# Kernel optimization log

Measured on AMD Instinct MI355X. Metric: run time of the kernel, lower is better.

The kernel has to match this reference:

```python
import jax, jax.numpy as jnp
import numpy as np

B, L, DN, DE, DD, H = 2, 512, 512, 128, 128, 8
DK, DEH, DDH = DN // H, DE // H, DD // H
F = 2 * DK + DEH + 2 * DDH  # per-head concat feature size (176)
SLOPE = 0.2


def _kaiming(key, out_f, in_f):
    bound = np.sqrt(6.0 / ((1.0 + SLOPE ** 2) * in_f))
    return jax.random.uniform(key, (out_f, in_f), minval=-bound, maxval=bound, dtype=jnp.float32)


def lin(x, w, b):
    y = jnp.einsum('...i,oi->...o', x, w)
    return y if b is None else y + b


def setup_inputs() -> dict:
    key = jax.random.key(0)
    ks = jax.random.split(key, 16)
    inp = {
        'node_representation': jax.random.normal(ks[0], (B, L, DN), dtype=jnp.float32),
        'edge_representation': jax.random.normal(ks[1], (B, L, L, DE), dtype=jnp.float32),
        'diff_vec': jax.random.normal(ks[2], (B, L, DD), dtype=jnp.float32),
        'Wn_w': _kaiming(ks[3], DN, DN), 'Wn_b': jnp.zeros((DN,), jnp.float32),
        'We_w': _kaiming(ks[4], DE, DE), 'We_b': jnp.zeros((DE,), jnp.float32),
        'Wd_w': _kaiming(ks[5], DD, DD), 'Wd_b': jnp.zeros((DD,), jnp.float32),
        'Wh_w': _kaiming(ks[6], DK, DK), 'Wh_b': jnp.zeros((DK,), jnp.float32),
        'attn_w': _kaiming(ks[7], 1, F),
        'outn_w': _kaiming(ks[8], DN, DN), 'outn_b': jnp.zeros((DN,), jnp.float32),
        'Wn2_w': _kaiming(ks[9], DN, DN), 'Wn2_b': jnp.zeros((DN,), jnp.float32),
        'We2_w': _kaiming(ks[10], DE, DE), 'We2_b': jnp.zeros((DE,), jnp.float32),
        'Wd2_w': _kaiming(ks[11], DD, DD), 'Wd2_b': jnp.zeros((DD,), jnp.float32),
        'edge_w': _kaiming(ks[12], DEH, F), 'edge_b': jnp.zeros((DEH,), jnp.float32),
        'oute_w': _kaiming(ks[13], DE, DE), 'oute_b': jnp.zeros((DE,), jnp.float32),
    }
    return inp


def reference(node_representation, edge_representation, diff_vec,
              Wn_w, Wn_b, We_w, We_b, Wd_w, Wd_b, Wh_w, Wh_b, attn_w,
              outn_w, outn_b, Wn2_w, Wn2_b, We2_w, We2_b, Wd2_w, Wd2_b,
              edge_w, edge_b, oute_w, oute_b):
    lrelu = lambda x: jax.nn.leaky_relu(x, SLOPE)

    # ---- node update (GAT-style with concat score decomposed per term) ----
    npj = lin(node_representation, Wn_w, Wn_b).reshape(B, L, H, DK)
    epj = lin(edge_representation, We_w, We_b).reshape(B, L, L, H, DEH)
    dpj = lin(diff_vec, Wd_w, Wd_b).reshape(B, L, H, DDH)
    a = attn_w[0]  # concat order: [hi, hj, edge, di, dj]
    a_hi, a_hj = a[:DK], a[DK:2 * DK]
    a_e = a[2 * DK:2 * DK + DEH]
    a_di, a_dj = a[2 * DK + DEH:2 * DK + DEH + DDH], a[-DDH:]
    # scores[b,i,j,h]
    s = (jnp.einsum('blhd,d->blh', npj, a_hi)[:, :, None, :]
         + jnp.einsum('blhd,d->blh', npj, a_hj)[:, None, :, :]
         + jnp.einsum('blmhe,e->blmh', epj, a_e)
         + jnp.einsum('blhd,d->blh', dpj, a_di)[:, :, None, :]
         + jnp.einsum('blhd,d->blh', dpj, a_dj)[:, None, :, :])
    diag = jnp.eye(L, dtype=bool)[None, :, :, None]
    s = jnp.where(diag, -jnp.inf, s)
    probs = jax.nn.softmax(lrelu(s), axis=2)  # softmax over j
    node_wh = lin(npj, Wh_w, Wh_b)  # [B,L,H,DK]
    agg = jnp.einsum('blmh,bmhd->blhd', probs, node_wh)
    new_node = (npj + lrelu(agg)).reshape(B, L, DN)
    new_node = lin(new_node, outn_w, outn_b)

    # ---- edge update (concat-linear decomposed into per-term matmuls) ----
    np2 = lin(new_node, Wn2_w, Wn2_b).reshape(B, L, H, DK)
    ep2 = lin(edge_representation, We2_w, We2_b).reshape(B, L, L, H, DEH)
    dp2 = lin(diff_vec, Wd2_w, Wd2_b).reshape(B, L, H, DDH)
    # edge concat order: [edge, hi, hj, di, dj]
    W_e = edge_w[:, :DEH]
    W_hi = edge_w[:, DEH:DEH + DK]
    W_hj = edge_w[:, DEH + DK:DEH + 2 * DK]
    W_di = edge_w[:, DEH + 2 * DK:DEH + 2 * DK + DDH]
    W_dj = edge_w[:, -DDH:]
    e_out = (jnp.einsum('blmhe,fe->blmhf', ep2, W_e)
             + jnp.einsum('blhd,fd->blhf', np2, W_hi)[:, :, None]
             + jnp.einsum('blhd,fd->blhf', np2, W_hj)[:, None]
             + jnp.einsum('blhd,fd->blhf', dp2, W_di)[:, :, None]
             + jnp.einsum('blhd,fd->blhf', dp2, W_dj)[:, None]
             + edge_b)
    new_edge = lin(e_out.reshape(B, L, L, DE), oute_w, oute_b)
    return new_node, new_edge
```

## Files before the change

kernel.cpp:

```cpp
#include <hip/hip_runtime.h>
#include <hip/hip_bf16.h>

typedef unsigned short u16;
typedef unsigned short u16x8 __attribute__((ext_vector_type(8)));
typedef __bf16 bf16x8 __attribute__((ext_vector_type(8)));
typedef float f32x4 __attribute__((ext_vector_type(4)));

#define LRS 0.2f

__device__ __forceinline__ float bf2f(u16 u) { return __uint_as_float(((unsigned)u) << 16); }
__device__ __forceinline__ u16 f2b(float f) {
  __hip_bfloat16 h = __float2bfloat16(f);
  return __builtin_bit_cast(u16, h);
}

template<int K, int O, int KSEG>
__device__ __forceinline__ void gemm_rows4(const float* xr, const float* W, const float* bias,
                                           float* yl, float* yg, int ygstride) {
  constexpr int KPT = K / KSEG;
  constexpr int OPP = 256 / KSEG;
  const int t = threadIdx.x;
  const int ks = t % KSEG;
  const int oi = t / KSEG;
#pragma unroll
  for (int pass = 0; pass < O / OPP; ++pass) {
    const int o = pass * OPP + oi;
    float a0 = 0, a1 = 0, a2 = 0, a3 = 0;
    const float* wp = W + (size_t)o * K + ks * KPT;
    const float* xb = xr + ks * KPT;
#pragma unroll 4
    for (int kc = 0; kc < KPT; kc += 4) {
      f32x4 w4 = *(const f32x4*)(wp + kc);
      f32x4 x0 = *(const f32x4*)(xb + kc);
      f32x4 x1 = *(const f32x4*)(xb + K + kc);
      f32x4 x2 = *(const f32x4*)(xb + 2 * K + kc);
      f32x4 x3 = *(const f32x4*)(xb + 3 * K + kc);
#pragma unroll
      for (int j = 0; j < 4; ++j) {
        float w = w4[j];
        a0 += x0[j] * w;
        a1 += x1[j] * w;
        a2 += x2[j] * w;
        a3 += x3[j] * w;
      }
    }
#pragma unroll
    for (int d = 1; d < KSEG; d <<= 1) {
      a0 += __shfl_xor(a0, d, 64);
      a1 += __shfl_xor(a1, d, 64);
      a2 += __shfl_xor(a2, d, 64);
      a3 += __shfl_xor(a3, d, 64);
    }
    if (ks == 0) {
      float bv = bias ? bias[o] : 0.0f;
      float v0 = a0 + bv, v1 = a1 + bv, v2 = a2 + bv, v3 = a3 + bv;
      if (yl) { yl[o] = v0; yl[O + o] = v1; yl[2 * O + o] = v2; yl[3 * O + o] = v3; }
      if (yg) { yg[o] = v0; yg[ygstride + o] = v1; yg[2 * (size_t)ygstride + o] = v2; yg[3 * (size_t)ygstride + o] = v3; }
    }
  }
}

__global__ __launch_bounds__(256) void kW1(const float* We_w, const float* We_b, const float* attn,
                                           const float* We2_w, const float* We2_b,
                                           const float* edge_w, const float* edge_b,
                                           float* Mfull, float* vf, float* cbe, float* sconst) {
  int gid = blockIdx.x * 256 + threadIdx.x;
  if (gid < 16384) {
    int hf = gid >> 7, c = gid & 127;
    int h = hf >> 4, fo = hf & 15;
    float s = 0;
    for (int e = 0; e < 16; ++e)
      s += edge_w[fo * 176 + e] * We2_w[(h * 16 + e) * 128 + c];
    Mfull[hf * 128 + c] = s;
  } else if (gid < 16384 + 2048) {
    int idx = gid - 16384;
    int c = idx >> 4, hc = idx & 15;
    if (hc < 8) {
      float s = 0;
      for (int e = 0; e < 16; ++e)
        s += We_w[(hc * 16 + e) * 128 + c] * attn[128 + e];
      vf[c * 8 + hc] = s;
    }
  } else if (gid < 18432 + 128) {
    int hf = gid - 18432;
    int h = hf >> 4, fo = hf & 15;
    float s = edge_b[fo];
    for (int e = 0; e < 16; ++e)
      s += We2_b[h * 16 + e] * edge_w[fo * 176 + e];
    cbe[hf] = s;
  } else if (gid < 18560 + 8) {
    int h = gid - 18560;
    float s = 0;
    for (int e = 0; e < 16; ++e)
      s += We_b[h * 16 + e] * attn[128 + e];
    sconst[h] = s;
  }
}

__global__ __launch_bounds__(256) void kW2(const float* oute_w, const float* Mfull, u16* Gb) {
  int gid = blockIdx.x * 256 + threadIdx.x;
  int o = gid >> 7, c = gid & 127;
  float s = 0;
  for (int k = 0; k < 128; ++k)
    s += oute_w[o * 128 + k] * Mfull[k * 128 + c];
  Gb[o * 128 + c] = f2b(s);
}

__global__ __launch_bounds__(256) void kN1(const float* node, const float* diff,
                                           const float* Wn_w, const float* Wn_b,
                                           const float* Wd_w, const float* Wd_b,
                                           const float* Wh_w, const float* Wh_b,
                                           const float* attn, const float* sconst,
                                           float* npj_g, float* nwh_g,
                                           float* srow_g, float* scol_g) {
  __shared__ float nrow[4 * 512], npjl[4 * 512], drow[4 * 128], dpjl[4 * 128];
  const int t = threadIdx.x;
  const int r0 = blockIdx.x * 4;
  *(f32x4*)&nrow[t * 8]     = *(const f32x4*)(node + (size_t)r0 * 512 + t * 8);
  *(f32x4*)&nrow[t * 8 + 4] = *(const f32x4*)(node + (size_t)r0 * 512 + t * 8 + 4);
  if (t < 64) {
    *(f32x4*)&drow[t * 8]     = *(const f32x4*)(diff + (size_t)r0 * 128 + t * 8);
    *(f32x4*)&drow[t * 8 + 4] = *(const f32x4*)(diff + (size_t)r0 * 128 + t * 8 + 4);
  }
  __syncthreads();
  gemm_rows4<512, 512, 4>(nrow, Wn_w, Wn_b, npjl, npj_g + (size_t)r0 * 512, 512);
  gemm_rows4<128, 128, 4>(drow, Wd_w, Wd_b, dpjl, nullptr, 0);
  __syncthreads();
  {
    int d = t & 63, hh = t >> 6;
#pragma unroll
    for (int hi = 0; hi < 2; ++hi) {
      int h = hh + hi * 4;
      float wb = Wh_b[d];
      float acc[4] = {wb, wb, wb, wb};
      for (int k = 0; k < 64; ++k) {
        float w = Wh_w[d * 64 + k];
#pragma unroll
        for (int r = 0; r < 4; ++r) acc[r] += npjl[r * 512 + h * 64 + k] * w;
      }
#pragma unroll
      for (int r = 0; r < 4; ++r) nwh_g[(size_t)(r0 + r) * 512 + h * 64 + d] = acc[r];
    }
  }
  if (t < 32) {
    int r = t >> 3, h = t & 7;
    float shi = 0, shj = 0, sdi = 0, sdj = 0;
    for (int d = 0; d < 64; ++d) {
      float x = npjl[r * 512 + h * 64 + d];
      shi += x * attn[d];
      shj += x * attn[64 + d];
    }
    for (int e = 0; e < 16; ++e) {
      float x = dpjl[r * 128 + h * 16 + e];
      sdi += x * attn[144 + e];
      sdj += x * attn[160 + e];
    }
    srow_g[(r0 + r) * 8 + h] = shi + sdi + sconst[h];
    scol_g[(r0 + r) * 8 + h] = shj + sdj;
  }
}

__global__ __launch_bounds__(256) void kA(const float* edge, const float* npj, const float* nwh,
                                          const float* srow, const float* scol,
                                          const float* vf, float* nnp) {
  __shared__ float sm[4608];
  __shared__ u16 Pb[4][512][8];
  __shared__ float red[256];
  __shared__ float mxh8[8];
  __shared__ float inv8v[4][8];
  const int blk = blockIdx.x;
  const int b = blk >> 7, lt = blk & 127;
  const int t = threadIdx.x;
  const int sub = t & 15, rg = t >> 4;
  const int h = t & 7, seg = t >> 3;

  f32x4 vrx[16];
#pragma unroll
  for (int q = 0; q < 16; ++q) vrx[q] = *(const f32x4*)(vf + sub * 64 + q * 4);

  for (int li = 0; li < 4; ++li) {
    const int l = lt * 4 + li;
    const size_t bl = (size_t)b * 512 + l;
    const float* ebase = edge + (bl * 512 + rg) * 128 + sub * 8;
    f32x4 a0v, a1v, b0v, b1v;
    a0v = *(const f32x4*)ebase;             a1v = *(const f32x4*)(ebase + 4);
    b0v = *(const f32x4*)(ebase + 2048);    b1v = *(const f32x4*)(ebase + 2052);
#define SCORE_ROW(C0, C1, IT)                                                  \
    {                                                                          \
      float acc[8];                                                            \
      _Pragma("unroll") for (int h2 = 0; h2 < 8; ++h2) acc[h2] = 0.0f;         \
      _Pragma("unroll") for (int j = 0; j < 4; ++j) {                          \
        _Pragma("unroll") for (int h2 = 0; h2 < 8; ++h2) {                     \
          acc[h2] += C0[j] * vrx[j * 2 + (h2 >> 2)][h2 & 3];                   \
          acc[h2] += C1[j] * vrx[8 + j * 2 + (h2 >> 2)][h2 & 3];               \
        }                                                                      \
      }                                                                        \
      _Pragma("unroll") for (int d = 1; d < 16; d <<= 1) {                     \
        _Pragma("unroll") for (int h2 = 0; h2 < 8; ++h2)                       \
          acc[h2] += __shfl_xor(acc[h2], d, 64);                               \
      }                                                                        \
      if (sub < 8) {                                                           \
        float a = acc[0];                                                      \
        _Pragma("unroll") for (int h2 = 1; h2 < 8; ++h2)                       \
          if (sub == h2) a = acc[h2];                                          \
        sm[(IT * 16 + rg) * 9 + sub] = a;                                      \
      }                                                                        \
    }
    for (int it = 0; it < 32; it += 2) {
      SCORE_ROW(a0v, a1v, it);
      if (it + 2 < 32) {
        const float* p = ebase + (size_t)(it + 2) * 2048;
        a0v = *(const f32x4*)p; a1v = *(const f32x4*)(p + 4);
      }
      SCORE_ROW(b0v, b1v, (it + 1));
      if (it + 3 < 32) {
        const float* p = ebase + (size_t)(it + 3) * 2048;
        b0v = *(const f32x4*)p; b1v = *(const f32x4*)(p + 4);
      }
    }
#undef SCORE_ROW
    __syncthreads();
    const float srh2 = srow[bl * 8 + h];
    float mx = -__builtin_inff();
#pragma unroll 4
    for (int i = 0; i < 16; ++i) {
      int m = seg * 16 + i;
      float sv = sm[m * 9 + h] + srh2 + scol[((size_t)b * 512 + m) * 8 + h];
      sv = (m == l) ? -__builtin_inff() : (sv >= 0.0f ? sv : LRS * sv);
      sm[m * 9 + h] = sv;
      mx = fmaxf(mx, sv);
    }
    red[t] = mx;
    __syncthreads();
    if (t < 8) {
      float m2 = -__builtin_inff();
      for (int sg = 0; sg < 32; ++sg) m2 = fmaxf(m2, red[sg * 8 + t]);
      mxh8[t] = m2;
    }
    __syncthreads();
    float mh = mxh8[h];
    float smv = 0;
#pragma unroll 4
    for (int i = 0; i < 16; ++i) {
      int m = seg * 16 + i;
      float p = __expf(sm[m * 9 + h] - mh);
      Pb[li][m][h] = f2b(p);
      smv += p;
    }
    red[t] = smv;
    __syncthreads();
    if (t < 8) {
      float s2 = 0;
      for (int sg = 0; sg < 32; ++sg) s2 += red[sg * 8 + t];
      inv8v[li][t] = 1.0f / s2;
    }
    __syncthreads();
  }

  const int half = t >> 7, oq = t & 127;
  const int o4 = oq * 4, hh = oq >> 4;
  f32x4 acc[4] = {};
  const float* nb = nwh + (size_t)b * 512 * 512;
  for (int m = half * 256; m < half * 256 + 256; ++m) {
    f32x4 nv = *(const f32x4*)(nb + (size_t)m * 512 + o4);
#pragma unroll
    for (int li = 0; li < 4; ++li)
      acc[li] += bf2f(Pb[li][m][hh]) * nv;
  }
#pragma unroll
  for (int li = 0; li < 4; ++li)
    *(f32x4*)&sm[(half * 4 + li) * 512 + o4] = acc[li];
  __syncthreads();
  if (t < 128) {
    int ob = t * 4, h2 = t >> 4;
#pragma unroll
    for (int li = 0; li < 4; ++li) {
      f32x4 s0 = *(f32x4*)&sm[li * 512 + ob];
      f32x4 s1 = *(f32x4*)&sm[(4 + li) * 512 + ob];
      const size_t bl = (size_t)b * 512 + lt * 4 + li;
      f32x4 np4 = *(const f32x4*)(npj + bl * 512 + ob);
      float iv = inv8v[li][h2];
      f32x4 o;
#pragma unroll
      for (int j = 0; j < 4; ++j) {
        float a = (s0[j] + s1[j]) * iv;
        a = a >= 0.0f ? a : LRS * a;
        o[j] = np4[j] + a;
      }
      *(f32x4*)(nnp + bl * 512 + ob) = o;
    }
  }
}

__global__ __launch_bounds__(256) void kN2(const float* nnp, const float* outn_w, const float* outn_b,
                                           float* out0) {
  __shared__ float xr[4 * 512];
  const int t = threadIdx.x;
  const int r0 = blockIdx.x * 4;
  *(f32x4*)&xr[t * 4]        = *(const f32x4*)(nnp + (size_t)r0 * 512 + t * 4);
  *(f32x4*)&xr[1024 + t * 4] = *(const f32x4*)(nnp + (size_t)r0 * 512 + 1024 + t * 4);
  __syncthreads();
  gemm_rows4<512, 512, 4>(xr, outn_w, outn_b, nullptr, out0 + (size_t)r0 * 512, 512);
}

__global__ __launch_bounds__(256) void kN34(const float* nn, const float* diff,
                                            const float* Wn2_w, const float* Wn2_b,
                                            const float* Wd2_w, const float* Wd2_b,
                                            const float* edge_w, const float* cbe,
                                            const float* oute_w, const float* oute_b,
                                            float* Pl, float* Pm) {
  __shared__ float xr[4 * 512], np2l[4 * 512], dr[4 * 128], dp2l[4 * 128];
  __shared__ float Rls[4 * 128], Rms[4 * 128];
  const int t = threadIdx.x;
  const int r0 = blockIdx.x * 4;
  *(f32x4*)&xr[t * 4]        = *(const f32x4*)(nn + (size_t)r0 * 512 + t * 4);
  *(f32x4*)&xr[1024 + t * 4] = *(const f32x4*)(nn + (size_t)r0 * 512 + 1024 + t * 4);
  if (t < 64) {
    *(f32x4*)&dr[t * 8]     = *(const f32x4*)(diff + (size_t)r0 * 128 + t * 8);
    *(f32x4*)&dr[t * 8 + 4] = *(const f32x4*)(diff + (size_t)r0 * 128 + t * 8 + 4);
  }
  __syncthreads();
  gemm_rows4<512, 512, 4>(xr, Wn2_w, Wn2_b, np2l, nullptr, 0);
  gemm_rows4<128, 128, 4>(dr, Wd2_w, Wd2_b, dp2l, nullptr, 0);
  __syncthreads();
  {
    int hf = t & 127, which = t >> 7;
    int h = hf >> 4, fo = hf & 15;
    const float* wh = edge_w + fo * 176 + 16 + which * 64;
    const float* wd = edge_w + fo * 176 + 144 + which * 16;
    float add = which ? 0.0f : cbe[hf];
    float* dst = which ? Rms : Rls;
#pragma unroll
    for (int r = 0; r < 4; ++r) {
      float a = add;
      for (int d = 0; d < 64; ++d) a += np2l[r * 512 + h * 64 + d] * wh[d];
      for (int e = 0; e < 16; ++e) a += dp2l[r * 128 + h * 16 + e] * wd[e];
      dst[r * 128 + hf] = a;
    }
  }
  __syncthreads();
  gemm_rows4<128, 128, 4>(Rls, oute_w, oute_b, nullptr, Pl + (size_t)r0 * 128, 128);
  gemm_rows4<128, 128, 4>(Rms, oute_w, nullptr, nullptr, Pm + (size_t)r0 * 128, 128);
}

__global__ __launch_bounds__(256) void kE(const float* edge, const u16* Gb,
                                          const float* Pl, const float* Pm, float* oute) {
  __shared__ u16 Gt[16384];
  __shared__ u16 At[8192];
  const int tile = blockIdx.x;
  const int bl = tile >> 2;
  const int b = bl >> 9;
  const int q0 = (tile & 3) * 128;
  const int t = threadIdx.x, lane = t & 63, w = t >> 6;
#pragma unroll
  for (int i2 = 0; i2 < 8; ++i2) {
    int u = i2 * 256 + t;
    int row = u >> 4, cu = u & 15;
    *(u16x8*)(Gt + (row * 16 + (cu ^ (row & 7))) * 8) = *(const u16x8*)(Gb + u * 8);
  }
  const int wr = w >> 1, wc = w & 1;
  const int colL = lane & 15, kg = lane >> 4;
  const float* plp = Pl + (size_t)bl * 128;
  float plv[4];
#pragma unroll
  for (int n = 0; n < 4; ++n) plv[n] = plp[wc * 64 + n * 16 + colL];
  const int arow = t >> 2, aseg = t & 3;

  for (int sub = 0; sub < 2; ++sub) {
    const int r0 = q0 + sub * 64;
    {
      const float* p = edge + ((size_t)bl * 512 + r0 + arow) * 128 + aseg * 32;
      f32x4 v[8];
#pragma unroll
      for (int q = 0; q < 8; ++q) v[q] = *(const f32x4*)(p + q * 4);
#pragma unroll
      for (int jj = 0; jj < 4; ++jj) {
        u16x8 a8;
#pragma unroll
        for (int j2 = 0; j2 < 4; ++j2) {
          a8[j2]     = f2b(v[2 * jj][j2]);
          a8[4 + j2] = f2b(v[2 * jj + 1][j2]);
        }
        int cu = aseg * 4 + jj;
        *(u16x8*)(At + (arow * 16 + (cu ^ (arow & 7))) * 8) = a8;
      }
    }
    __syncthreads();
    f32x4 acc[2][4] = {};
#pragma unroll
    for (int ks = 0; ks < 4; ++ks) {
      int cu = ks * 4 + kg;
      bf16x8 af[2], bfv[4];
#pragma unroll
      for (int i = 0; i < 2; ++i) {
        int row = wr * 32 + i * 16 + colL;
        af[i] = *(bf16x8*)(At + (row * 16 + (cu ^ (row & 7))) * 8);
      }
#pragma unroll
      for (int n = 0; n < 4; ++n) {
        int orow = wc * 64 + n * 16 + colL;
        bfv[n] = *(bf16x8*)(Gt + (orow * 16 + (cu ^ (orow & 7))) * 8);
      }
#pragma unroll
      for (int i = 0; i < 2; ++i)
#pragma unroll
        for (int n = 0; n < 4; ++n)
          acc[i][n] = __builtin_amdgcn_mfma_f32_16x16x32_bf16(af[i], bfv[n], acc[i][n], 0, 0, 0);
    }
    float* ob = oute + ((size_t)bl * 512 + r0) * 128;
#pragma unroll
    for (int i = 0; i < 2; ++i) {
#pragma unroll
      for (int r = 0; r < 4; ++r) {
        int m = wr * 32 + i * 16 + kg * 4 + r;
        const float* pmp = Pm + ((size_t)b * 512 + r0 + m) * 128;
#pragma unroll
        for (int n = 0; n < 4; ++n) {
          int o = wc * 64 + n * 16 + colL;
          ob[(size_t)m * 128 + o] = acc[i][n][r] + plv[n] + pmp[o];
        }
      }
    }
    __syncthreads();
  }
}

extern "C" void kernel_launch(void* const* d_in, const int* in_sizes, int n_in,
                              void* d_out, int out_size, void* d_ws, size_t ws_size,
                              hipStream_t stream) {
  (void)in_sizes; (void)n_in; (void)out_size; (void)ws_size;
  const float* node   = (const float*)d_in[0];
  const float* edge   = (const float*)d_in[1];
  const float* diff   = (const float*)d_in[2];
  const float* Wn_w   = (const float*)d_in[3];
  const float* Wn_b   = (const float*)d_in[4];
  const float* We_w   = (const float*)d_in[5];
  const float* We_b   = (const float*)d_in[6];
  const float* Wd_w   = (const float*)d_in[7];
  const float* Wd_b   = (const float*)d_in[8];
  const float* Wh_w   = (const float*)d_in[9];
  const float* Wh_b   = (const float*)d_in[10];
  const float* attn   = (const float*)d_in[11];
  const float* outn_w = (const float*)d_in[12];
  const float* outn_b = (const float*)d_in[13];
  const float* Wn2_w  = (const float*)d_in[14];
  const float* Wn2_b  = (const float*)d_in[15];
  const float* We2_w  = (const float*)d_in[16];
  const float* We2_b  = (const float*)d_in[17];
  const float* Wd2_w  = (const float*)d_in[18];
  const float* Wd2_b  = (const float*)d_in[19];
  const float* edge_w = (const float*)d_in[20];
  const float* edge_b = (const float*)d_in[21];
  const float* oute_w = (const float*)d_in[22];
  const float* oute_b = (const float*)d_in[23];

  float* out0 = (float*)d_out;
  float* out1 = out0 + 524288;

  float* f = (float*)d_ws;
  size_t off = 0;
  auto alloc = [&](size_t n) { float* p = f + off; off += (n + 7) & ~(size_t)7; return p; };
  float* npj    = alloc(524288);
  float* nwh    = alloc(524288);
  float* srow   = alloc(8192);
  float* scol   = alloc(8192);
  float* sconst = alloc(8);
  float* cbe    = alloc(128);
  float* Mfull  = alloc(16384);
  float* nnp    = alloc(524288);
  float* Pl     = alloc(131072);
  float* Pm     = alloc(131072);
  float* vf     = alloc(1024);
  u16* Gb = (u16*)(f + off); off += 8192;

  hipLaunchKernelGGL(kW1, dim3(73), dim3(256), 0, stream,
                     We_w, We_b, attn, We2_w, We2_b, edge_w, edge_b, Mfull, vf, cbe, sconst);
  hipLaunchKernelGGL(kW2, dim3(64), dim3(256), 0, stream, oute_w, Mfull, Gb);
  hipLaunchKernelGGL(kN1, dim3(256), dim3(256), 0, stream,
                     node, diff, Wn_w, Wn_b, Wd_w, Wd_b, Wh_w, Wh_b, attn, sconst,
                     npj, nwh, srow, scol);
  hipLaunchKernelGGL(kA, dim3(256), dim3(256), 0, stream,
                     edge, npj, nwh, srow, scol, vf, nnp);
  hipLaunchKernelGGL(kN2, dim3(256), dim3(256), 0, stream, nnp, outn_w, outn_b, out0);
  hipLaunchKernelGGL(kN34, dim3(256), dim3(256), 0, stream,
                     out0, diff, Wn2_w, Wn2_b, Wd2_w, Wd2_b, edge_w, cbe, oute_w, oute_b, Pl, Pm);
  hipLaunchKernelGGL(kE, dim3(4096), dim3(256), 0, stream, edge, Gb, Pl, Pm, out1);
}
```

Measured before the change: 472.7 us.

## Shrink per-block rows, fuse kN2 into kN34, and vectorize kE epilogue stores

Node-level kernels now handle 2 rows per block instead of 4, and the attention kernel handles one query row per block, so those launches use 2-4x more blocks to fill the GPU better. The outn projection (kN2) is merged into the following Wn2/Wd2 kernel, which removes one launch and a global round trip for the hidden rows. Attention probabilities stay in fp32 shared memory instead of being packed to bf16. In the edge kernel the MFMA operands are swapped so each lane holds four consecutive output columns, letting the epilogue use vector loads and stores. The cost is that weight matrices are reread by twice as many blocks, and the node-weighted sum in kA rereads nwh for every single row instead of sharing it across four.

Result: faster. 458.7 us (-3.0%).

```diff
diff --git a/kernel.cpp b/kernel.cpp
--- a/kernel.cpp
+++ b/kernel.cpp
@@ -8,14 +8,13 @@
 
 #define LRS 0.2f
 
-__device__ __forceinline__ float bf2f(u16 u) { return __uint_as_float(((unsigned)u) << 16); }
 __device__ __forceinline__ u16 f2b(float f) {
   __hip_bfloat16 h = __float2bfloat16(f);
   return __builtin_bit_cast(u16, h);
 }
 
-template<int K, int O, int KSEG>
-__device__ __forceinline__ void gemm_rows4(const float* xr, const float* W, const float* bias,
+template<int K, int O, int KSEG, int R>
+__device__ __forceinline__ void gemm_rowsR(const float* xr, const float* W, const float* bias,
                                            float* yl, float* yg, int ygstride) {
   constexpr int KPT = K / KSEG;
   constexpr int OPP = 256 / KSEG;
@@ -25,37 +24,33 @@
 #pragma unroll
   for (int pass = 0; pass < O / OPP; ++pass) {
     const int o = pass * OPP + oi;
-    float a0 = 0, a1 = 0, a2 = 0, a3 = 0;
+    float a[R];
+#pragma unroll
+    for (int r = 0; r < R; ++r) a[r] = 0.0f;
     const float* wp = W + (size_t)o * K + ks * KPT;
     const float* xb = xr + ks * KPT;
 #pragma unroll 4
     for (int kc = 0; kc < KPT; kc += 4) {
       f32x4 w4 = *(const f32x4*)(wp + kc);
-      f32x4 x0 = *(const f32x4*)(xb + kc);
-      f32x4 x1 = *(const f32x4*)(xb + K + kc);
-      f32x4 x2 = *(const f32x4*)(xb + 2 * K + kc);
-      f32x4 x3 = *(const f32x4*)(xb + 3 * K + kc);
-#pragma unroll
-      for (int j = 0; j < 4; ++j) {
-        float w = w4[j];
-        a0 += x0[j] * w;
-        a1 += x1[j] * w;
-        a2 += x2[j] * w;
-        a3 += x3[j] * w;
-      }
-    }
-#pragma unroll
-    for (int d = 1; d < KSEG; d <<= 1) {
-      a0 += __shfl_xor(a0, d, 64);
-      a1 += __shfl_xor(a1, d, 64);
-      a2 += __shfl_xor(a2, d, 64);
-      a3 += __shfl_xor(a3, d, 64);
-    }
+#pragma unroll
+      for (int r = 0; r < R; ++r) {
+        f32x4 x = *(const f32x4*)(xb + r * K + kc);
+#pragma unroll
+        for (int j = 0; j < 4; ++j) a[r] += x[j] * w4[j];
+      }
+    }
+#pragma unroll
+    for (int d = 1; d < KSEG; d <<= 1)
+#pragma unroll
+      for (int r = 0; r < R; ++r) a[r] += __shfl_xor(a[r], d, 64);
     if (ks == 0) {
       float bv = bias ? bias[o] : 0.0f;
-      float v0 = a0 + bv, v1 = a1 + bv, v2 = a2 + bv, v3 = a3 + bv;
-      if (yl) { yl[o] = v0; yl[O + o] = v1; yl[2 * O + o] = v2; yl[3 * O + o] = v3; }
-      if (yg) { yg[o] = v0; yg[ygstride + o] = v1; yg[2 * (size_t)ygstride + o] = v2; yg[3 * (size_t)ygstride + o] = v3; }
+#pragma unroll
+      for (int r = 0; r < R; ++r) {
+        float v = a[r] + bv;
+        if (yl) yl[r * O + o] = v;
+        if (yg) yg[(size_t)r * ygstride + o] = v;
+      }
     }
   }
 }
@@ -113,18 +108,14 @@
                                            const float* attn, const float* sconst,
                                            float* npj_g, float* nwh_g,
                                            float* srow_g, float* scol_g) {
-  __shared__ float nrow[4 * 512], npjl[4 * 512], drow[4 * 128], dpjl[4 * 128];
+  __shared__ float nrow[2 * 512], npjl[2 * 512], drow[2 * 128], dpjl[2 * 128];
   const int t = threadIdx.x;
-  const int r0 = blockIdx.x * 4;
-  *(f32x4*)&nrow[t * 8]     = *(const f32x4*)(node + (size_t)r0 * 512 + t * 8);
-  *(f32x4*)&nrow[t * 8 + 4] = *(const f32x4*)(node + (size_t)r0 * 512 + t * 8 + 4);
-  if (t < 64) {
-    *(f32x4*)&drow[t * 8]     = *(const f32x4*)(diff + (size_t)r0 * 128 + t * 8);
-    *(f32x4*)&drow[t * 8 + 4] = *(const f32x4*)(diff + (size_t)r0 * 128 + t * 8 + 4);
-  }
-  __syncthreads();
-  gemm_rows4<512, 512, 4>(nrow, Wn_w, Wn_b, npjl, npj_g + (size_t)r0 * 512, 512);
-  gemm_rows4<128, 128, 4>(drow, Wd_w, Wd_b, dpjl, nullptr, 0);
+  const int r0 = blockIdx.x * 2;
+  *(f32x4*)&nrow[t * 4] = *(const f32x4*)(node + (size_t)r0 * 512 + t * 4);
+  if (t < 64) *(f32x4*)&drow[t * 4] = *(const f32x4*)(diff + (size_t)r0 * 128 + t * 4);
+  __syncthreads();
+  gemm_rowsR<512, 512, 4, 2>(nrow, Wn_w, Wn_b, npjl, npj_g + (size_t)r0 * 512, 512);
+  gemm_rowsR<128, 128, 4, 2>(drow, Wd_w, Wd_b, dpjl, nullptr, 0);
   __syncthreads();
   {
     int d = t & 63, hh = t >> 6;
@@ -132,17 +123,17 @@
     for (int hi = 0; hi < 2; ++hi) {
       int h = hh + hi * 4;
       float wb = Wh_b[d];
-      float acc[4] = {wb, wb, wb, wb};
+      float acc[2] = {wb, wb};
       for (int k = 0; k < 64; ++k) {
         float w = Wh_w[d * 64 + k];
 #pragma unroll
-        for (int r = 0; r < 4; ++r) acc[r] += npjl[r * 512 + h * 64 + k] * w;
-      }
-#pragma unroll
-      for (int r = 0; r < 4; ++r) nwh_g[(size_t)(r0 + r) * 512 + h * 64 + d] = acc[r];
-    }
-  }
-  if (t < 32) {
+        for (int r = 0; r < 2; ++r) acc[r] += npjl[r * 512 + h * 64 + k] * w;
+      }
+#pragma unroll
+      for (int r = 0; r < 2; ++r) nwh_g[(size_t)(r0 + r) * 512 + h * 64 + d] = acc[r];
+    }
+  }
+  if (t < 16) {
     int r = t >> 3, h = t & 7;
     float shi = 0, shj = 0, sdi = 0, sdj = 0;
     for (int d = 0; d < 64; ++d) {
@@ -164,12 +155,11 @@
                                           const float* srow, const float* scol,
                                           const float* vf, float* nnp) {
   __shared__ float sm[4608];
-  __shared__ u16 Pb[4][512][8];
+  __shared__ float part[2][512];
   __shared__ float red[256];
-  __shared__ float mxh8[8];
-  __shared__ float inv8v[4][8];
-  const int blk = blockIdx.x;
-  const int b = blk >> 7, lt = blk & 127;
+  __shared__ float mxh8[8], inv8[8];
+  const int bl = blockIdx.x;
+  const int b = bl >> 9, l = bl & 511;
   const int t = threadIdx.x;
   const int sub = t & 15, rg = t >> 4;
   const int h = t & 7, seg = t >> 3;
@@ -178,13 +168,11 @@
 #pragma unroll
   for (int q = 0; q < 16; ++q) vrx[q] = *(const f32x4*)(vf + sub * 64 + q * 4);
 
-  for (int li = 0; li < 4; ++li) {
-    const int l = lt * 4 + li;
-    const size_t bl = (size_t)b * 512 + l;
-    const float* ebase = edge + (bl * 512 + rg) * 128 + sub * 8;
+  {
+    const float* ebase = edge + ((size_t)bl * 512 + rg) * 128 + sub * 8;
     f32x4 a0v, a1v, b0v, b1v;
-    a0v = *(const f32x4*)ebase;             a1v = *(const f32x4*)(ebase + 4);
-    b0v = *(const f32x4*)(ebase + 2048);    b1v = *(const f32x4*)(ebase + 2052);
+    a0v = *(const f32x4*)ebase;          a1v = *(const f32x4*)(ebase + 4);
+    b0v = *(const f32x4*)(ebase + 2048); b1v = *(const f32x4*)(ebase + 2052);
 #define SCORE_ROW(C0, C1, IT)                                                  \
     {                                                                          \
       float acc[8];                                                            \
@@ -219,109 +207,88 @@
       }
     }
 #undef SCORE_ROW
-    __syncthreads();
-    const float srh2 = srow[bl * 8 + h];
-    float mx = -__builtin_inff();
+  }
+  __syncthreads();
+  const float srh2 = srow[(size_t)bl * 8 + h];
+  float mx = -__builtin_inff();
 #pragma unroll 4
-    for (int i = 0; i < 16; ++i) {
-      int m = seg * 16 + i;
-      float sv = sm[m * 9 + h] + srh2 + scol[((size_t)b * 512 + m) * 8 + h];
-      sv = (m == l) ? -__builtin_inff() : (sv >= 0.0f ? sv : LRS * sv);
-      sm[m * 9 + h] = sv;
-      mx = fmaxf(mx, sv);
-    }
-    red[t] = mx;
-    __syncthreads();
-    if (t < 8) {
-      float m2 = -__builtin_inff();
-      for (int sg = 0; sg < 32; ++sg) m2 = fmaxf(m2, red[sg * 8 + t]);
-      mxh8[t] = m2;
-    }
-    __syncthreads();
-    float mh = mxh8[h];
-    float smv = 0;
+  for (int i = 0; i < 16; ++i) {
+    int m = seg * 16 + i;
+    float sv = sm[m * 9 + h] + srh2 + scol[((size_t)b * 512 + m) * 8 + h];
+    sv = (m == l) ? -__builtin_inff() : (sv >= 0.0f ? sv : LRS * sv);
+    sm[m * 9 + h] = sv;
+    mx = fmaxf(mx, sv);
+  }
+  red[t] = mx;
+  __syncthreads();
+  if (t < 8) {
+    float m2 = -__builtin_inff();
+    for (int sg = 0; sg < 32; ++sg) m2 = fmaxf(m2, red[sg * 8 + t]);
+    mxh8[t] = m2;
+  }
+  __syncthreads();
+  float mh = mxh8[h];
+  float smv = 0;
 #pragma unroll 4
-    for (int i = 0; i < 16; ++i) {
-      int m = seg * 16 + i;
-      float p = __expf(sm[m * 9 + h] - mh);
-      Pb[li][m][h] = f2b(p);
-      smv += p;
-    }
-    red[t] = smv;
-    __syncthreads();
-    if (t < 8) {
-      float s2 = 0;
-      for (int sg = 0; sg < 32; ++sg) s2 += red[sg * 8 + t];
-      inv8v[li][t] = 1.0f / s2;
-    }
-    __syncthreads();
-  }
-
+  for (int i = 0; i < 16; ++i) {
+    int m = seg * 16 + i;
+    float p = __expf(sm[m * 9 + h] - mh);
+    sm[m * 9 + h] = p;
+    smv += p;
+  }
+  red[t] = smv;
+  __syncthreads();
+  if (t < 8) {
+    float s2 = 0;
+    for (int sg = 0; sg < 32; ++sg) s2 += red[sg * 8 + t];
+    inv8[t] = 1.0f / s2;
+  }
+  __syncthreads();
   const int half = t >> 7, oq = t & 127;
   const int o4 = oq * 4, hh = oq >> 4;
-  f32x4 acc[4] = {};
+  f32x4 acc4a = {0, 0, 0, 0}, acc4b = {0, 0, 0, 0};
   const float* nb = nwh + (size_t)b * 512 * 512;
-  for (int m = half * 256; m < half * 256 + 256; ++m) {
-    f32x4 nv = *(const f32x4*)(nb + (size_t)m * 512 + o4);
-#pragma unroll
-    for (int li = 0; li < 4; ++li)
-      acc[li] += bf2f(Pb[li][m][hh]) * nv;
-  }
-#pragma unroll
-  for (int li = 0; li < 4; ++li)
-    *(f32x4*)&sm[(half * 4 + li) * 512 + o4] = acc[li];
+  for (int m = half * 256; m < half * 256 + 256; m += 2) {
+    acc4a += sm[m * 9 + hh]       * *(const f32x4*)(nb + (size_t)m * 512 + o4);
+    acc4b += sm[(m + 1) * 9 + hh] * *(const f32x4*)(nb + (size_t)(m + 1) * 512 + o4);
+  }
+  *(f32x4*)&part[half][o4] = acc4a + acc4b;
   __syncthreads();
   if (t < 128) {
     int ob = t * 4, h2 = t >> 4;
-#pragma unroll
-    for (int li = 0; li < 4; ++li) {
-      f32x4 s0 = *(f32x4*)&sm[li * 512 + ob];
-      f32x4 s1 = *(f32x4*)&sm[(4 + li) * 512 + ob];
-      const size_t bl = (size_t)b * 512 + lt * 4 + li;
-      f32x4 np4 = *(const f32x4*)(npj + bl * 512 + ob);
-      float iv = inv8v[li][h2];
-      f32x4 o;
-#pragma unroll
-      for (int j = 0; j < 4; ++j) {
-        float a = (s0[j] + s1[j]) * iv;
-        a = a >= 0.0f ? a : LRS * a;
-        o[j] = np4[j] + a;
-      }
-      *(f32x4*)(nnp + bl * 512 + ob) = o;
-    }
-  }
-}
-
-__global__ __launch_bounds__(256) void kN2(const float* nnp, const float* outn_w, const float* outn_b,
-                                           float* out0) {
-  __shared__ float xr[4 * 512];
+    f32x4 s0 = *(f32x4*)&part[0][ob];
+    f32x4 s1 = *(f32x4*)&part[1][ob];
+    f32x4 np4 = *(const f32x4*)(npj + (size_t)bl * 512 + ob);
+    float iv = inv8[h2];
+    f32x4 o;
+#pragma unroll
+    for (int j = 0; j < 4; ++j) {
+      float a = (s0[j] + s1[j]) * iv;
+      a = a >= 0.0f ? a : LRS * a;
+      o[j] = np4[j] + a;
+    }
+    *(f32x4*)(nnp + (size_t)bl * 512 + ob) = o;
+  }
+}
+
+__global__ __launch_bounds__(256) void kN234(const float* nnp, const float* diff,
+                                             const float* outn_w, const float* outn_b,
+                                             const float* Wn2_w, const float* Wn2_b,
+                                             const float* Wd2_w, const float* Wd2_b,
+                                             const float* edge_w, const float* cbe,
+                                             const float* oute_w, const float* oute_b,
+                                             float* out0, float* Pl, float* Pm) {
+  __shared__ float xr[2 * 512], o0l[2 * 512], np2l[2 * 512], dr[2 * 128], dp2l[2 * 128];
+  __shared__ float Rls[2 * 128], Rms[2 * 128];
   const int t = threadIdx.x;
-  const int r0 = blockIdx.x * 4;
-  *(f32x4*)&xr[t * 4]        = *(const f32x4*)(nnp + (size_t)r0 * 512 + t * 4);
-  *(f32x4*)&xr[1024 + t * 4] = *(const f32x4*)(nnp + (size_t)r0 * 512 + 1024 + t * 4);
-  __syncthreads();
-  gemm_rows4<512, 512, 4>(xr, outn_w, outn_b, nullptr, out0 + (size_t)r0 * 512, 512);
-}
-
-__global__ __launch_bounds__(256) void kN34(const float* nn, const float* diff,
-                                            const float* Wn2_w, const float* Wn2_b,
-                                            const float* Wd2_w, const float* Wd2_b,
-                                            const float* edge_w, const float* cbe,
-                                            const float* oute_w, const float* oute_b,
-                                            float* Pl, float* Pm) {
-  __shared__ float xr[4 * 512], np2l[4 * 512], dr[4 * 128], dp2l[4 * 128];
-  __shared__ float Rls[4 * 128], Rms[4 * 128];
-  const int t = threadIdx.x;
-  const int r0 = blockIdx.x * 4;
-  *(f32x4*)&xr[t * 4]        = *(const f32x4*)(nn + (size_t)r0 * 512 + t * 4);
-  *(f32x4*)&xr[1024 + t * 4] = *(const f32x4*)(nn + (size_t)r0 * 512 + 1024 + t * 4);
-  if (t < 64) {
-    *(f32x4*)&dr[t * 8]     = *(const f32x4*)(diff + (size_t)r0 * 128 + t * 8);
-    *(f32x4*)&dr[t * 8 + 4] = *(const f32x4*)(diff + (size_t)r0 * 128 + t * 8 + 4);
-  }
-  __syncthreads();
-  gemm_rows4<512, 512, 4>(xr, Wn2_w, Wn2_b, np2l, nullptr, 0);
-  gemm_rows4<128, 128, 4>(dr, Wd2_w, Wd2_b, dp2l, nullptr, 0);
+  const int r0 = blockIdx.x * 2;
+  *(f32x4*)&xr[t * 4] = *(const f32x4*)(nnp + (size_t)r0 * 512 + t * 4);
+  if (t < 64) *(f32x4*)&dr[t * 4] = *(const f32x4*)(diff + (size_t)r0 * 128 + t * 4);
+  __syncthreads();
+  gemm_rowsR<512, 512, 4, 2>(xr, outn_w, outn_b, o0l, out0 + (size_t)r0 * 512, 512);
+  gemm_rowsR<128, 128, 4, 2>(dr, Wd2_w, Wd2_b, dp2l, nullptr, 0);
+  __syncthreads();
+  gemm_rowsR<512, 512, 4, 2>(o0l, Wn2_w, Wn2_b, np2l, nullptr, 0);
   __syncthreads();
   {
     int hf = t & 127, which = t >> 7;
@@ -331,7 +298,7 @@
     float add = which ? 0.0f : cbe[hf];
     float* dst = which ? Rms : Rls;
 #pragma unroll
-    for (int r = 0; r < 4; ++r) {
+    for (int r = 0; r < 2; ++r) {
       float a = add;
       for (int d = 0; d < 64; ++d) a += np2l[r * 512 + h * 64 + d] * wh[d];
       for (int e = 0; e < 16; ++e) a += dp2l[r * 128 + h * 16 + e] * wd[e];
@@ -339,8 +306,8 @@
     }
   }
   __syncthreads();
-  gemm_rows4<128, 128, 4>(Rls, oute_w, oute_b, nullptr, Pl + (size_t)r0 * 128, 128);
-  gemm_rows4<128, 128, 4>(Rms, oute_w, nullptr, nullptr, Pm + (size_t)r0 * 128, 128);
+  gemm_rowsR<128, 128, 4, 2>(Rls, oute_w, oute_b, nullptr, Pl + (size_t)r0 * 128, 128);
+  gemm_rowsR<128, 128, 4, 2>(Rms, oute_w, nullptr, nullptr, Pm + (size_t)r0 * 128, 128);
 }
 
 __global__ __launch_bounds__(256) void kE(const float* edge, const u16* Gb,
@@ -361,9 +328,9 @@
   const int wr = w >> 1, wc = w & 1;
   const int colL = lane & 15, kg = lane >> 4;
   const float* plp = Pl + (size_t)bl * 128;
-  float plv[4];
-#pragma unroll
-  for (int n = 0; n < 4; ++n) plv[n] = plp[wc * 64 + n * 16 + colL];
+  f32x4 plv4[4];
+#pragma unroll
+  for (int n = 0; n < 4; ++n) plv4[n] = *(const f32x4*)(plp + wc * 64 + n * 16 + kg * 4);
   const int arow = t >> 2, aseg = t & 3;
 
   for (int sub = 0; sub < 2; ++sub) {
@@ -405,20 +372,22 @@
       for (int i = 0; i < 2; ++i)
 #pragma unroll
         for (int n = 0; n < 4; ++n)
-          acc[i][n] = __builtin_amdgcn_mfma_f32_16x16x32_bf16(af[i], bfv[n], acc[i][n], 0, 0, 0);
+          acc[i][n] = __builtin_amdgcn_mfma_f32_16x16x32_bf16(bfv[n], af[i], acc[i][n], 0, 0, 0);
     }
     float* ob = oute + ((size_t)bl * 512 + r0) * 128;
 #pragma unroll
     for (int i = 0; i < 2; ++i) {
-#pragma unroll
-      for (int r = 0; r < 4; ++r) {
-        int m = wr * 32 + i * 16 + kg * 4 + r;
-        const float* pmp = Pm + ((size_t)b * 512 + r0 + m) * 128;
-#pragma unroll
-        for (int n = 0; n < 4; ++n) {
-          int o = wc * 64 + n * 16 + colL;
-          ob[(size_t)m * 128 + o] = acc[i][n][r] + plv[n] + pmp[o];
-        }
+      int m = wr * 32 + i * 16 + colL;
+      const float* pmp = Pm + ((size_t)b * 512 + r0 + m) * 128;
+      float* orow = ob + (size_t)m * 128;
+#pragma unroll
+      for (int n = 0; n < 4; ++n) {
+        int oc = wc * 64 + n * 16 + kg * 4;
+        f32x4 pm4 = *(const f32x4*)(pmp + oc);
+        f32x4 o4;
+#pragma unroll
+        for (int r = 0; r < 4; ++r) o4[r] = acc[i][n][r] + plv4[n][r] + pm4[r];
+        *(f32x4*)(orow + oc) = o4;
       }
     }
     __syncthreads();
@@ -476,13 +445,13 @@
   hipLaunchKernelGGL(kW1, dim3(73), dim3(256), 0, stream,
                      We_w, We_b, attn, We2_w, We2_b, edge_w, edge_b, Mfull, vf, cbe, sconst);
   hipLaunchKernelGGL(kW2, dim3(64), dim3(256), 0, stream, oute_w, Mfull, Gb);
-  hipLaunchKernelGGL(kN1, dim3(256), dim3(256), 0, stream,
+  hipLaunchKernelGGL(kN1, dim3(512), dim3(256), 0, stream,
                      node, diff, Wn_w, Wn_b, Wd_w, Wd_b, Wh_w, Wh_b, attn, sconst,
                      npj, nwh, srow, scol);
-  hipLaunchKernelGGL(kA, dim3(256), dim3(256), 0, stream,
+  hipLaunchKernelGGL(kA, dim3(1024), dim3(256), 0, stream,
                      edge, npj, nwh, srow, scol, vf, nnp);
-  hipLaunchKernelGGL(kN2, dim3(256), dim3(256), 0, stream, nnp, outn_w, outn_b, out0);
-  hipLaunchKernelGGL(kN34, dim3(256), dim3(256), 0, stream,
-                     out0, diff, Wn2_w, Wn2_b, Wd2_w, Wd2_b, edge_w, cbe, oute_w, oute_b, Pl, Pm);
+  hipLaunchKernelGGL(kN234, dim3(512), dim3(256), 0, stream,
+                     nnp, diff, outn_w, outn_b, Wn2_w, Wn2_b, Wd2_w, Wd2_b,
+                     edge_w, cbe, oute_w, oute_b, out0, Pl, Pm);
   hipLaunchKernelGGL(kE, dim3(4096), dim3(256), 0, stream, edge, Gb, Pl, Pm, out1);
 }
```
